# Kernel tuning notes

Measured on AMD Instinct MI355X. Metric: run time of the kernel, lower is better.

The kernel has to match this reference:

```python
import jax, jax.numpy as jnp
import numpy as np

EPS = 1e-12  # torch F.normalize default eps


def setup_inputs() -> dict:
    key = jax.random.key(0)
    k1, k2, k3 = jax.random.split(key, 3)
    ns, d_in, n_feat, n_classes = 16384, 512, 256, 1000
    x = jax.random.normal(k1, (ns, d_in), dtype=jnp.float32)
    W = jax.random.normal(k2, (d_in, n_feat), dtype=jnp.float32) * 0.05
    # class prototypes: L2-normalized embeddings, one per seen class (seen_c == n_classes)
    means = jax.random.normal(k3, (n_classes, n_feat), dtype=jnp.float32)
    means = means / jnp.maximum(jnp.linalg.norm(means, axis=1, keepdims=True), EPS)
    return {"x": x, "W": W, "means": means, "t": 0}


def reference(x, W, means, t):
    # forward_training: backbone + L2 normalization along feature dim
    feats = x @ W                                   # [ns, n_feat]
    preds = feats / jnp.maximum(jnp.linalg.norm(feats, axis=1, keepdims=True), EPS)
    # deployment forward: nearest prototype by negative dot product
    # original: per-sample dist = -means @ pred^T; dist.min(0) -> class index
    dist = -(preds @ means.T)                       # [ns, seen_c]
    classpred = jnp.argmin(dist, axis=1)            # first min on ties, matches torch
    n_classes = means.shape[0]
    out = jax.nn.one_hot(classpred, n_classes, dtype=jnp.float32)  # [ns, n_classes]
    return out
```

## Files before the change

### kernel.cpp

```cpp
#include <hip/hip_runtime.h>
#include <float.h>

#define NS   16384
#define K1   512
#define F    256
#define NC   1000
#define SPB  32
#define NTHR 512
#define NBLK (NS / SPB)


typedef _Float16 half8 __attribute__((ext_vector_type(8)));
typedef float    float4v __attribute__((ext_vector_type(4)));

#define WH_OFF 0
#define WL_OFF 131072
#define MH_OFF 262144
#define ML_OFF (262144 + 262144)

__global__ void prep_w(const float* __restrict__ W, _Float16* __restrict__ ws) {
    int g    = blockIdx.x * blockDim.x + threadIdx.x;
    int lane = g & 63, tile = g >> 6;
    int ks = tile >> 4, nt = tile & 15;
    int k0 = ks * 32 + (lane >> 4) * 8;
    int n  = nt * 16 + (lane & 15);
    _Float16 h[8], l[8];
#pragma unroll
    for (int j = 0; j < 8; ++j) {
        float v = W[(size_t)(k0 + j) * F + n] * 16.0f;
        _Float16 hi = (_Float16)v;
        h[j] = hi;
        l[j] = (_Float16)(v - (float)hi);
    }
    _Float16* dh = ws + WH_OFF + (size_t)g * 8;
    _Float16* dl = ws + WL_OFF + (size_t)g * 8;
#pragma unroll
    for (int j = 0; j < 8; ++j) { dh[j] = h[j]; dl[j] = l[j]; }
}

__global__ void prep_m(const float* __restrict__ means, _Float16* __restrict__ ws) {
    int g    = blockIdx.x * blockDim.x + threadIdx.x;
    int lane = g & 63, tile = g >> 6;
    int ks = tile >> 6, gt = tile & 63;
    int k0 = ks * 32 + (lane >> 4) * 8;
    int c  = gt * 16 + (lane & 15);
    _Float16 h[8], l[8];
#pragma unroll
    for (int j = 0; j < 8; ++j) {
        float v = (c < NC) ? means[(size_t)c * F + k0 + j] * 16.0f : 0.0f;
        _Float16 hi = (_Float16)v;
        h[j] = hi;
        l[j] = (_Float16)(v - (float)hi);
    }
    _Float16* dh = ws + MH_OFF + (size_t)g * 8;
    _Float16* dl = ws + ML_OFF + (size_t)g * 8;
#pragma unroll
    for (int j = 0; j < 8; ++j) { dh[j] = h[j]; dl[j] = l[j]; }
}

#define MFMA(a, b, c) __builtin_amdgcn_mfma_f32_16x16x32_f16((a), (b), (c), 0, 0, 0)

__attribute__((amdgpu_flat_work_group_size(NTHR, NTHR), amdgpu_waves_per_eu(2, 4)))
__global__ void fused_mfma(const float* __restrict__ x,
                           const _Float16* __restrict__ ws,
                           float* __restrict__ out) {
    __shared__ _Float16 xsh[2][32][44];
    __shared__ _Float16 xsl[2][32][44];
    __shared__ _Float16 fh[32][264];
    __shared__ _Float16 fl[32][264];
    __shared__ float cand_v[32][8];
    __shared__ int   cand_i[32][8];
    __shared__ int   bidx[32];

    const int tid  = threadIdx.x;
    const int lane = tid & 63;
    const int w    = tid >> 6;
    const int quad = lane >> 4;
    const int cl   = lane & 15;
    const int s0   = blockIdx.x * SPB;

    const int xrow = tid >> 4;
    const int xc   = (tid & 15) * 2;

    float4v acc1[2][2];
#pragma unroll
    for (int p = 0; p < 2; ++p)
#pragma unroll
        for (int mt = 0; mt < 2; ++mt)
            acc1[p][mt] = (float4v){0.f, 0.f, 0.f, 0.f};

    float2 xv = *reinterpret_cast<const float2*>(x + (size_t)(s0 + xrow) * K1 + xc);

    for (int ks = 0; ks < 16; ++ks) {
        const int buf = ks & 1;
        {
            float vx = xv.x * 8.0f, vy = xv.y * 8.0f;
            _Float16 hx = (_Float16)vx, hy = (_Float16)vy;
            xsh[buf][xrow][xc]     = hx;
            xsh[buf][xrow][xc + 1] = hy;
            xsl[buf][xrow][xc]     = (_Float16)(vx - (float)hx);
            xsl[buf][xrow][xc + 1] = (_Float16)(vy - (float)hy);
        }
        __syncthreads();
        if (ks < 15)
            xv = *reinterpret_cast<const float2*>(
                x + (size_t)(s0 + xrow) * K1 + (ks + 1) * 32 + xc);

        half8 ah[2], al[2];
#pragma unroll
        for (int mt = 0; mt < 2; ++mt) {
            ah[mt] = *reinterpret_cast<const half8*>(&xsh[buf][mt * 16 + cl][quad * 8]);
            al[mt] = *reinterpret_cast<const half8*>(&xsl[buf][mt * 16 + cl][quad * 8]);
        }
#pragma unroll
        for (int p = 0; p < 2; ++p) {
            const int tile = ks * 16 + (w * 2 + p);
            half8 bh = *reinterpret_cast<const half8*>(
                ws + WH_OFF + ((size_t)tile * 64 + lane) * 8);
            half8 bl = *reinterpret_cast<const half8*>(
                ws + WL_OFF + ((size_t)tile * 64 + lane) * 8);
#pragma unroll
            for (int mt = 0; mt < 2; ++mt) {
                acc1[p][mt] = MFMA(ah[mt], bh, acc1[p][mt]);
                acc1[p][mt] = MFMA(ah[mt], bl, acc1[p][mt]);
                acc1[p][mt] = MFMA(al[mt], bh, acc1[p][mt]);
            }
        }
    }

#pragma unroll
    for (int p = 0; p < 2; ++p)
#pragma unroll
        for (int mt = 0; mt < 2; ++mt)
#pragma unroll
            for (int r = 0; r < 4; ++r) {
                int srow = mt * 16 + quad * 4 + r;
                int n    = (w * 2 + p) * 16 + cl;
                float v  = acc1[p][mt][r];
                _Float16 hi = (_Float16)v;
                fh[srow][n] = hi;
                fl[srow][n] = (_Float16)(v - (float)hi);
            }
    __syncthreads();

    float4v acc2[2][8];
#pragma unroll
    for (int mt = 0; mt < 2; ++mt)
#pragma unroll
        for (int nt = 0; nt < 8; ++nt)
            acc2[mt][nt] = (float4v){0.f, 0.f, 0.f, 0.f};

    for (int ks = 0; ks < 8; ++ks) {
        half8 fah[2], fal[2];
#pragma unroll
        for (int mt = 0; mt < 2; ++mt) {
            fah[mt] = *reinterpret_cast<const half8*>(
                &fh[mt * 16 + cl][ks * 32 + quad * 8]);
            fal[mt] = *reinterpret_cast<const half8*>(
                &fl[mt * 16 + cl][ks * 32 + quad * 8]);
        }
#pragma unroll
        for (int nt = 0; nt < 8; ++nt) {
            const int tile = ks * 64 + (w * 8 + nt);
            half8 mh = *reinterpret_cast<const half8*>(
                ws + MH_OFF + ((size_t)tile * 64 + lane) * 8);
            half8 ml = *reinterpret_cast<const half8*>(
                ws + ML_OFF + ((size_t)tile * 64 + lane) * 8);
#pragma unroll
            for (int mt = 0; mt < 2; ++mt) {
                acc2[mt][nt] = MFMA(fah[mt], mh, acc2[mt][nt]);
                acc2[mt][nt] = MFMA(fah[mt], ml, acc2[mt][nt]);
                acc2[mt][nt] = MFMA(fal[mt], mh, acc2[mt][nt]);
            }
        }
    }

#pragma unroll
    for (int mt = 0; mt < 2; ++mt)
#pragma unroll
        for (int r = 0; r < 4; ++r) {
            float v  = -FLT_MAX;
            int   ix = 0x7FFFFFFF;
#pragma unroll
            for (int nt = 0; nt < 8; ++nt) {
                int c = (w * 8 + nt) * 16 + cl;
                if (c < NC) {
                    float sc = acc2[mt][nt][r];
                    if (sc > v) { v = sc; ix = c; }
                }
            }
#pragma unroll
            for (int off = 1; off < 16; off <<= 1) {
                float ov = __shfl_xor(v, off, 64);
                int   oi = __shfl_xor(ix, off, 64);
                if (ov > v || (ov == v && oi < ix)) { v = ov; ix = oi; }
            }
            if (cl == 0) {
                int srow = mt * 16 + quad * 4 + r;
                cand_v[srow][w] = v;
                cand_i[srow][w] = ix;
            }
        }
    __syncthreads();

    if (tid < 32) {
        float v  = cand_v[tid][0];
        int   ix = cand_i[tid][0];
#pragma unroll
        for (int q = 1; q < 8; ++q) {
            float ov = cand_v[tid][q];
            int   oi = cand_i[tid][q];
            if (ov > v || (ov == v && oi < ix)) { v = ov; ix = oi; }
        }
        bidx[tid] = ix;
    }
    __syncthreads();

    const int NF4 = NC / 4;
    for (int q = tid; q < SPB * NF4; q += NTHR) {
        int row   = q / NF4;
        int c4    = q - row * NF4;
        int b     = bidx[row];
        int cbase = c4 * 4;
        float4 v;
        v.x = (cbase + 0 == b) ? 1.f : 0.f;
        v.y = (cbase + 1 == b) ? 1.f : 0.f;
        v.z = (cbase + 2 == b) ? 1.f : 0.f;
        v.w = (cbase + 3 == b) ? 1.f : 0.f;
        *reinterpret_cast<float4*>(out + (size_t)(s0 + row) * NC + cbase) = v;
    }
}

extern "C" void kernel_launch(void* const* d_in, const int* in_sizes, int n_in,
                              void* d_out, int out_size, void* d_ws, size_t ws_size,
                              hipStream_t stream) {
    const float* x     = (const float*)d_in[0];
    const float* W     = (const float*)d_in[1];
    const float* means = (const float*)d_in[2];
    float* out         = (float*)d_out;
    _Float16* ws       = (_Float16*)d_ws;

    prep_w<<<64, 256, 0, stream>>>(W, ws);
    prep_m<<<128, 256, 0, stream>>>(means, ws);
    fused_mfma<<<NBLK, NTHR, 0, stream>>>(x, ws, out);
}
```

Before: 137.6 us.

## Interleave zero-fill of output with GEMM2 and merge prep kernels

The one-hot output is now zero-filled with float4 stores spread across the second GEMM's k-loop, so the 64MB output write overlaps MFMA compute instead of running as a separate tail phase. After the argmin, each sample's single 1.0 is written with a scattered store. The two weight-prep kernels are merged into one launch to cut launch overhead. The risk is extra store traffic competing with the fragment loads inside the GEMM loop.

```diff
diff --git a/kernel.cpp b/kernel.cpp
--- a/kernel.cpp
+++ b/kernel.cpp
@@ -18,44 +18,40 @@
 #define MH_OFF 262144
 #define ML_OFF (262144 + 262144)
 
-__global__ void prep_w(const float* __restrict__ W, _Float16* __restrict__ ws) {
-    int g    = blockIdx.x * blockDim.x + threadIdx.x;
-    int lane = g & 63, tile = g >> 6;
-    int ks = tile >> 4, nt = tile & 15;
-    int k0 = ks * 32 + (lane >> 4) * 8;
-    int n  = nt * 16 + (lane & 15);
-    _Float16 h[8], l[8];
-#pragma unroll
-    for (int j = 0; j < 8; ++j) {
-        float v = W[(size_t)(k0 + j) * F + n] * 16.0f;
-        _Float16 hi = (_Float16)v;
-        h[j] = hi;
-        l[j] = (_Float16)(v - (float)hi);
-    }
-    _Float16* dh = ws + WH_OFF + (size_t)g * 8;
-    _Float16* dl = ws + WL_OFF + (size_t)g * 8;
-#pragma unroll
-    for (int j = 0; j < 8; ++j) { dh[j] = h[j]; dl[j] = l[j]; }
-}
-
-__global__ void prep_m(const float* __restrict__ means, _Float16* __restrict__ ws) {
-    int g    = blockIdx.x * blockDim.x + threadIdx.x;
-    int lane = g & 63, tile = g >> 6;
-    int ks = tile >> 6, gt = tile & 63;
-    int k0 = ks * 32 + (lane >> 4) * 8;
-    int c  = gt * 16 + (lane & 15);
-    _Float16 h[8], l[8];
-#pragma unroll
-    for (int j = 0; j < 8; ++j) {
-        float v = (c < NC) ? means[(size_t)c * F + k0 + j] * 16.0f : 0.0f;
-        _Float16 hi = (_Float16)v;
-        h[j] = hi;
-        l[j] = (_Float16)(v - (float)hi);
-    }
-    _Float16* dh = ws + MH_OFF + (size_t)g * 8;
-    _Float16* dl = ws + ML_OFF + (size_t)g * 8;
-#pragma unroll
-    for (int j = 0; j < 8; ++j) { dh[j] = h[j]; dl[j] = l[j]; }
+__global__ void prep_frags(const float* __restrict__ W,
+                           const float* __restrict__ means,
+                           _Float16* __restrict__ ws) {
+    int g = blockIdx.x * blockDim.x + threadIdx.x;
+    if (g < 16384) {
+        int lane = g & 63, tile = g >> 6;
+        int ks = tile >> 4, nt = tile & 15;
+        int k0 = ks * 32 + (lane >> 4) * 8;
+        int n  = nt * 16 + (lane & 15);
+        _Float16* dh = ws + WH_OFF + (size_t)g * 8;
+        _Float16* dl = ws + WL_OFF + (size_t)g * 8;
+#pragma unroll
+        for (int j = 0; j < 8; ++j) {
+            float v = W[(size_t)(k0 + j) * F + n] * 16.0f;
+            _Float16 hi = (_Float16)v;
+            dh[j] = hi;
+            dl[j] = (_Float16)(v - (float)hi);
+        }
+    } else {
+        int gm = g - 16384;
+        int lane = gm & 63, tile = gm >> 6;
+        int ks = tile >> 6, gt = tile & 63;
+        int k0 = ks * 32 + (lane >> 4) * 8;
+        int c  = gt * 16 + (lane & 15);
+        _Float16* dh = ws + MH_OFF + (size_t)gm * 8;
+        _Float16* dl = ws + ML_OFF + (size_t)gm * 8;
+#pragma unroll
+        for (int j = 0; j < 8; ++j) {
+            float v = (c < NC) ? means[(size_t)c * F + k0 + j] * 16.0f : 0.0f;
+            _Float16 hi = (_Float16)v;
+            dh[j] = hi;
+            dl[j] = (_Float16)(v - (float)hi);
+        }
+    }
 }
 
 #define MFMA(a, b, c) __builtin_amdgcn_mfma_f32_16x16x32_f16((a), (b), (c), 0, 0, 0)
@@ -150,7 +146,20 @@
         for (int nt = 0; nt < 8; ++nt)
             acc2[mt][nt] = (float4v){0.f, 0.f, 0.f, 0.f};
 
+    const float4 zero4 = make_float4(0.f, 0.f, 0.f, 0.f);
+
     for (int ks = 0; ks < 8; ++ks) {
+        {
+            int q0 = ks * 1024 + tid;
+            if (q0 < 8000)
+                *reinterpret_cast<float4*>(
+                    out + (size_t)(s0 + q0 / 250) * NC + (q0 % 250) * 4) = zero4;
+            int q1 = q0 + 512;
+            if (q1 < 8000)
+                *reinterpret_cast<float4*>(
+                    out + (size_t)(s0 + q1 / 250) * NC + (q1 % 250) * 4) = zero4;
+        }
+
         half8 fah[2], fal[2];
 #pragma unroll
         for (int mt = 0; mt < 2; ++mt) {
@@ -216,19 +225,8 @@
     }
     __syncthreads();
 
-    const int NF4 = NC / 4;
-    for (int q = tid; q < SPB * NF4; q += NTHR) {
-        int row   = q / NF4;
-        int c4    = q - row * NF4;
-        int b     = bidx[row];
-        int cbase = c4 * 4;
-        float4 v;
-        v.x = (cbase + 0 == b) ? 1.f : 0.f;
-        v.y = (cbase + 1 == b) ? 1.f : 0.f;
-        v.z = (cbase + 2 == b) ? 1.f : 0.f;
-        v.w = (cbase + 3 == b) ? 1.f : 0.f;
-        *reinterpret_cast<float4*>(out + (size_t)(s0 + row) * NC + cbase) = v;
-    }
+    if (tid < SPB)
+        out[(size_t)(s0 + tid) * NC + bidx[tid]] = 1.0f;
 }
 
 extern "C" void kernel_launch(void* const* d_in, const int* in_sizes, int n_in,
@@ -240,7 +238,6 @@
     float* out         = (float*)d_out;
     _Float16* ws       = (_Float16*)d_ws;
 
-    prep_w<<<64, 256, 0, stream>>>(W, ws);
-    prep_m<<<128, 256, 0, stream>>>(means, ws);
+    prep_frags<<<192, 256, 0, stream>>>(W, means, ws);
     fused_mfma<<<NBLK, NTHR, 0, stream>>>(x, ws, out);
 }
```

Measured after the change: 168.3 us. +22.3%, slower.
